# Performance work log

Hardware: AMD Instinct MI355X
Metric: run time of the kernel (lower is better)

The kernel has to match this reference:

```python
import jax, jax.numpy as jnp
import numpy as np

N, B, K, LATENT, HIDDEN, OUT = 100000, 256, 32, 64, 256, 32


def setup_inputs() -> dict:
    key = jax.random.key(0)
    ks = jax.random.split(key, 7)
    z = jax.random.normal(ks[0], (B, K, LATENT), dtype=jnp.float32)
    s = jax.random.uniform(ks[1], (N, K), dtype=jnp.float32)
    batch = jax.random.randint(ks[2], (N,), 0, B, dtype=jnp.int64)
    W1 = jax.random.normal(ks[3], (LATENT, HIDDEN), dtype=jnp.float32) / np.sqrt(LATENT)
    b1 = jnp.zeros((HIDDEN,), dtype=jnp.float32)
    W2 = jax.random.normal(ks[4], (HIDDEN, OUT), dtype=jnp.float32) / np.sqrt(HIDDEN)
    b2 = jnp.zeros((OUT,), dtype=jnp.float32)
    return {"z": z, "s": s, "batch": batch, "W1": W1, "b1": b1, "W2": W2, "b2": b2}


def reference(z, s, batch, W1, b1, W2, b2):
    # z: [B, K, L] per-graph cluster latents; batch: [N] node->graph; s: [N, K]
    z_gather = z[batch]                                  # [N, K, L]
    node_lat = jnp.einsum("nk,nkl->nl", s, z_gather)     # [N, L]
    h = jax.nn.relu(node_lat @ W1 + b1)                  # [N, HIDDEN]
    return h @ W2 + b2                                   # [N, OUT]
```

## Files before the change

### kernel.cpp

```cpp
#include <hip/hip_runtime.h>
#include <hip/hip_fp16.h>


using f16   = _Float16;
using f16x4 = __attribute__((ext_vector_type(4))) _Float16;
using f16x8 = __attribute__((ext_vector_type(8))) _Float16;
using f32x4 = __attribute__((ext_vector_type(4))) float;

constexpr int NN     = 100000;
constexpr int KK     = 32;
constexpr int LATENT = 64;
constexpr int HIDDEN = 256;
constexpr int OUTD   = 32;

constexpr int BLOCK   = 256;
constexpr int W2F_OFF = 16384;


__global__ __launch_bounds__(1024)
void prep(const float* __restrict__ W1,
          const float* __restrict__ W2,
          const int*   __restrict__ batch,
          f16* __restrict__ wsf,
          int* __restrict__ cnt,
          int* __restrict__ perm) {
    __shared__ int lcnt[256];
    __shared__ int lbase[256];
    const int t = threadIdx.x;
    if (t < 256) lcnt[t] = 0;

    const int gid = blockIdx.x * 1024 + t;
    if (gid < 16384) {
        const int j = gid & 7, lane = (gid >> 3) & 63, g = gid >> 9;
        const int ks = g & 1, nt = g >> 1;
        const int k = ks * 32 + (lane >> 4) * 8 + j;
        const int c = nt * 16 + (lane & 15);
        wsf[gid] = (f16)W1[k * HIDDEN + c];
    } else if (gid < 16384 + 8192) {
        const int g2 = gid - 16384;
        const int j = g2 & 7, lane = (g2 >> 3) & 63, g = g2 >> 9;
        const int ks = g & 7, nt2 = g >> 3;
        const int k = ks * 32 + (lane >> 4) * 8 + j;
        const int c = nt2 * 16 + (lane & 15);
        wsf[W2F_OFF + g2] = (f16)W2[k * OUTD + c];
    }
    __syncthreads();

    const int n0 = (blockIdx.x * 1024 + t) * 4;
    int bb[4], slot[4];
    const bool act = n0 < NN;
    if (act) {
        const int4 bv = *(const int4*)(batch + n0);
        bb[0] = bv.x; bb[1] = bv.y; bb[2] = bv.z; bb[3] = bv.w;
        #pragma unroll
        for (int i = 0; i < 4; ++i) slot[i] = atomicAdd(&lcnt[bb[i]], 1);
    }
    __syncthreads();
    if (t < 256 && lcnt[t] > 0) lbase[t] = atomicAdd(&cnt[t], lcnt[t]);
    __syncthreads();
    if (act) {
        #pragma unroll
        for (int i = 0; i < 4; ++i)
            perm[(bb[i] << 9) + lbase[bb[i]] + slot[i]] = n0 + i;
    }
}

__global__ __launch_bounds__(BLOCK, 7)
void gnn_decoder(const float* __restrict__ z,
                 const float* __restrict__ s,
                 const f16*   __restrict__ wsf,
                 const int*   __restrict__ cnt,
                 const int*   __restrict__ perm,
                 const float* __restrict__ b1,
                 const float* __restrict__ b2,
                 float*       __restrict__ out)
{
    __shared__ f16 zf[4][64][8];
    __shared__ f16 latlds[4][64][20];
    __shared__ f16 hcf[4][2][64][8];

    const int bg    = blockIdx.x >> 3;
    const int chunk = blockIdx.x & 7;
    const int cnt_c = cnt[bg] - chunk * 64;
    if (cnt_c <= 0) return;
    const int cn    = cnt_c < 64 ? cnt_c : 64;
    const int start = (bg << 9) + chunk * 64;

    const int t    = threadIdx.x;
    const int w    = t >> 6;
    const int lane = t & 63;
    const int lrow = lane & 15;
    const int quad = lane >> 4;

    {
        const float* zb = z + (size_t)bg * (KK * LATENT) + quad * 8 * LATENT
                        + w * 16 + lrow;
        f16x8 v;
        #pragma unroll
        for (int j = 0; j < 8; ++j) v[j] = (f16)zb[j * LATENT];
        *(f16x8*)&zf[w][lane][0] = v;
    }

    const int slot_l = w * 16 + lrow;
    const int pn = perm[start + (slot_l < cn ? slot_l : 0)];
    f16x8 sA;
    {
        const float4* sp = (const float4*)(s + (size_t)pn * KK + quad * 8);
        const float4 s0 = sp[0], s1 = sp[1];
        sA[0] = (f16)s0.x; sA[1] = (f16)s0.y; sA[2] = (f16)s0.z; sA[3] = (f16)s0.w;
        sA[4] = (f16)s1.x; sA[5] = (f16)s1.y; sA[6] = (f16)s1.z; sA[7] = (f16)s1.w;
    }
    __syncthreads();

    #pragma unroll
    for (int lt = 0; lt < 4; ++lt) {
        const f16x8 zB = *(const f16x8*)&zf[lt][lane][0];
        f32x4 D = (f32x4){0.f, 0.f, 0.f, 0.f};
        D = __builtin_amdgcn_mfma_f32_16x16x32_f16(sA, zB, D, 0, 0, 0);
        f16x4 dv;
        #pragma unroll
        for (int r = 0; r < 4; ++r) dv[r] = (f16)D[r];
        *(f16x4*)&latlds[w][lt * 16 + lrow][quad * 4] = dv;
    }
    __builtin_amdgcn_wave_barrier();

    f16x8 latB0, latB1;
    #pragma unroll
    for (int j = 0; j < 8; ++j) {
        latB0[j] = latlds[w][quad * 8 + j][lrow];
        latB1[j] = latlds[w][32 + quad * 8 + j][lrow];
    }

    const f16x8*  W1f = (const f16x8*)wsf;
    const f16x8*  W2f = (const f16x8*)(wsf + W2F_OFF);
    const float4* b1v = (const float4*)b1;

    f32x4 O0 = (f32x4){0.f, 0.f, 0.f, 0.f};
    f32x4 O1 = (f32x4){0.f, 0.f, 0.f, 0.f};

    #pragma unroll
    for (int ksH = 0; ksH < 8; ++ksH) {
        #pragma unroll
        for (int p = 0; p < 2; ++p) {
            const int ntA = ksH * 2 + p;
            f32x4 C = (f32x4){0.f, 0.f, 0.f, 0.f};
            C = __builtin_amdgcn_mfma_f32_16x16x32_f16(
                    W1f[(ntA * 2 + 0) * 64 + lane], latB0, C, 0, 0, 0);
            C = __builtin_amdgcn_mfma_f32_16x16x32_f16(
                    W1f[(ntA * 2 + 1) * 64 + lane], latB1, C, 0, 0, 0);
            const float4 bq = b1v[ntA * 4 + quad];
            f16x4 hv;
            hv[0] = (f16)fmaxf(C[0] + bq.x, 0.f);
            hv[1] = (f16)fmaxf(C[1] + bq.y, 0.f);
            hv[2] = (f16)fmaxf(C[2] + bq.z, 0.f);
            hv[3] = (f16)fmaxf(C[3] + bq.w, 0.f);
            *(f16x4*)&hcf[w][ksH & 1][(p * 2 + (quad >> 1)) * 16 + lrow][(quad & 1) * 4] = hv;
        }
        __builtin_amdgcn_wave_barrier();
        const f16x8 Ah = *(const f16x8*)&hcf[w][ksH & 1][lane][0];
        O0 = __builtin_amdgcn_mfma_f32_16x16x32_f16(Ah, W2f[(0 * 8 + ksH) * 64 + lane], O0, 0, 0, 0);
        O1 = __builtin_amdgcn_mfma_f32_16x16x32_f16(Ah, W2f[(1 * 8 + ksH) * 64 + lane], O1, 0, 0, 0);
    }

    {
        int pnr[4];
        #pragma unroll
        for (int r = 0; r < 4; ++r) {
            const int m = w * 16 + quad * 4 + r;
            pnr[r] = (m < cn) ? perm[start + m] : -1;
        }
        const float b2a = b2[lrow];
        const float b2b = b2[16 + lrow];
        #pragma unroll
        for (int r = 0; r < 4; ++r) {
            if (pnr[r] >= 0) {
                float* dst = out + (size_t)pnr[r] * OUTD;
                dst[lrow]      = O0[r] + b2a;
                dst[16 + lrow] = O1[r] + b2b;
            }
        }
    }
}

extern "C" void kernel_launch(void* const* d_in, const int* in_sizes, int n_in,
                              void* d_out, int out_size, void* d_ws, size_t ws_size,
                              hipStream_t stream) {
    const float* z     = (const float*)d_in[0];
    const float* s     = (const float*)d_in[1];
    const int*   batch = (const int*)d_in[2];
    const float* W1    = (const float*)d_in[3];
    const float* b1    = (const float*)d_in[4];
    const float* W2    = (const float*)d_in[5];
    const float* b2    = (const float*)d_in[6];
    float* out = (float*)d_out;

    f16* wsf  = (f16*)d_ws;
    int* cnt  = (int*)((char*)d_ws + 49152);
    int* perm = cnt + 256;

    hipMemsetAsync(cnt, 0, 256 * sizeof(int), stream);
    prep<<<25, 1024, 0, stream>>>(W1, W2, batch, wsf, cnt, perm);
    gnn_decoder<<<256 * 8, BLOCK, 0, stream>>>(z, s, wsf, cnt, perm, b1, b2, out);
}
```

Measured before the change: 109.5 us.

## Replace global atomic bucketing with per-block histograms and in-kernel prefix scan

The prep kernel now writes a per-block histogram and per-block segment slots instead of atomically reserving global offsets. This removes the memset launch and the second atomic phase. The decoder rebuilds segment starts with a wave prefix scan over 25 block counts, then locates each node's segment. Output node indices are obtained by shuffle instead of reloading perm. The risk is that per-block segment capacity is capped at 64 slots, so nodes beyond that in a segment would be silently dropped, and each decoder block pays extra scan and search work.

```diff
diff --git a/kernel.cpp b/kernel.cpp
--- a/kernel.cpp
+++ b/kernel.cpp
@@ -13,8 +13,10 @@
 constexpr int HIDDEN = 256;
 constexpr int OUTD   = 32;
 
-constexpr int BLOCK   = 256;
-constexpr int W2F_OFF = 16384;
+constexpr int BLOCK    = 256;
+constexpr int W2F_OFF  = 16384;
+constexpr int NPREP    = 25;
+constexpr int SEGCAP   = 64;
 
 
 __global__ __launch_bounds__(1024)
@@ -22,10 +24,9 @@
           const float* __restrict__ W2,
           const int*   __restrict__ batch,
           f16* __restrict__ wsf,
-          int* __restrict__ cnt,
-          int* __restrict__ perm) {
+          int* __restrict__ hist,
+          int* __restrict__ perm2) {
     __shared__ int lcnt[256];
-    __shared__ int lbase[256];
     const int t = threadIdx.x;
     if (t < 256) lcnt[t] = 0;
 
@@ -46,7 +47,7 @@
     }
     __syncthreads();
 
-    const int n0 = (blockIdx.x * 1024 + t) * 4;
+    const int n0 = gid * 4;
     int bb[4], slot[4];
     const bool act = n0 < NN;
     if (act) {
@@ -55,22 +56,22 @@
         #pragma unroll
         for (int i = 0; i < 4; ++i) slot[i] = atomicAdd(&lcnt[bb[i]], 1);
     }
+    if (act) {
+        #pragma unroll
+        for (int i = 0; i < 4; ++i)
+            if (slot[i] < SEGCAP)
+                perm2[(bb[i] * NPREP + blockIdx.x) * SEGCAP + slot[i]] = n0 + i;
+    }
     __syncthreads();
-    if (t < 256 && lcnt[t] > 0) lbase[t] = atomicAdd(&cnt[t], lcnt[t]);
-    __syncthreads();
-    if (act) {
-        #pragma unroll
-        for (int i = 0; i < 4; ++i)
-            perm[(bb[i] << 9) + lbase[bb[i]] + slot[i]] = n0 + i;
-    }
+    if (t < 256) hist[blockIdx.x * 256 + t] = lcnt[t];
 }
 
 __global__ __launch_bounds__(BLOCK, 7)
 void gnn_decoder(const float* __restrict__ z,
                  const float* __restrict__ s,
                  const f16*   __restrict__ wsf,
-                 const int*   __restrict__ cnt,
-                 const int*   __restrict__ perm,
+                 const int*   __restrict__ hist,
+                 const int*   __restrict__ perm2,
                  const float* __restrict__ b1,
                  const float* __restrict__ b2,
                  float*       __restrict__ out)
@@ -78,13 +79,10 @@
     __shared__ f16 zf[4][64][8];
     __shared__ f16 latlds[4][64][20];
     __shared__ f16 hcf[4][2][64][8];
+    __shared__ int sstart[26];
 
     const int bg    = blockIdx.x >> 3;
     const int chunk = blockIdx.x & 7;
-    const int cnt_c = cnt[bg] - chunk * 64;
-    if (cnt_c <= 0) return;
-    const int cn    = cnt_c < 64 ? cnt_c : 64;
-    const int start = (bg << 9) + chunk * 64;
 
     const int t    = threadIdx.x;
     const int w    = t >> 6;
@@ -101,8 +99,31 @@
         *(f16x8*)&zf[w][lane][0] = v;
     }
 
-    const int slot_l = w * 16 + lrow;
-    const int pn = perm[start + (slot_l < cn ? slot_l : 0)];
+    if (t < 64) {
+        const int c = (lane < NPREP) ? hist[lane * 256 + bg] : 0;
+        int x = c;
+        #pragma unroll
+        for (int o = 1; o < 32; o <<= 1) {
+            const int y = __shfl_up(x, o);
+            if (lane >= o) x += y;
+        }
+        if (lane < NPREP) sstart[lane] = x - c;
+        if (lane == NPREP - 1) sstart[NPREP] = x;
+    }
+    __syncthreads();
+
+    const int total = sstart[NPREP];
+    const int cnt_c = total - chunk * 64;
+    if (cnt_c <= 0) return;
+    const int cn = cnt_c < 64 ? cnt_c : 64;
+
+    int gs = chunk * 64 + w * 16 + lrow;
+    if (gs >= total) gs = total - 1;
+    int seg = 0;
+    #pragma unroll
+    for (int i = 1; i < NPREP; ++i) seg = (gs >= sstart[i]) ? i : seg;
+    const int pn = perm2[(bg * NPREP + seg) * SEGCAP + (gs - sstart[seg])];
+
     f16x8 sA;
     {
         const float4* sp = (const float4*)(s + (size_t)pn * KK + quad * 8);
@@ -110,7 +131,6 @@
         sA[0] = (f16)s0.x; sA[1] = (f16)s0.y; sA[2] = (f16)s0.z; sA[3] = (f16)s0.w;
         sA[4] = (f16)s1.x; sA[5] = (f16)s1.y; sA[6] = (f16)s1.z; sA[7] = (f16)s1.w;
     }
-    __syncthreads();
 
     #pragma unroll
     for (int lt = 0; lt < 4; ++lt) {
@@ -163,18 +183,14 @@
     }
 
     {
-        int pnr[4];
+        const float b2a = b2[lrow];
+        const float b2b = b2[16 + lrow];
         #pragma unroll
         for (int r = 0; r < 4; ++r) {
             const int m = w * 16 + quad * 4 + r;
-            pnr[r] = (m < cn) ? perm[start + m] : -1;
-        }
-        const float b2a = b2[lrow];
-        const float b2b = b2[16 + lrow];
-        #pragma unroll
-        for (int r = 0; r < 4; ++r) {
-            if (pnr[r] >= 0) {
-                float* dst = out + (size_t)pnr[r] * OUTD;
+            const int pr = __shfl(pn, quad * 4 + r);
+            if (m < cn) {
+                float* dst = out + (size_t)pr * OUTD;
                 dst[lrow]      = O0[r] + b2a;
                 dst[16 + lrow] = O1[r] + b2b;
             }
@@ -194,11 +210,10 @@
     const float* b2    = (const float*)d_in[6];
     float* out = (float*)d_out;
 
-    f16* wsf  = (f16*)d_ws;
-    int* cnt  = (int*)((char*)d_ws + 49152);
-    int* perm = cnt + 256;
-
-    hipMemsetAsync(cnt, 0, 256 * sizeof(int), stream);
-    prep<<<25, 1024, 0, stream>>>(W1, W2, batch, wsf, cnt, perm);
-    gnn_decoder<<<256 * 8, BLOCK, 0, stream>>>(z, s, wsf, cnt, perm, b1, b2, out);
+    f16* wsf   = (f16*)d_ws;
+    int* hist  = (int*)((char*)d_ws + 49152);
+    int* perm2 = hist + NPREP * 256;
+
+    prep<<<NPREP, 1024, 0, stream>>>(W1, W2, batch, wsf, hist, perm2);
+    gnn_decoder<<<256 * 8, BLOCK, 0, stream>>>(z, s, wsf, hist, perm2, b1, b2, out);
 }
```

After: 103.9 us. -5.2%, faster.
